# Kernel tuning notes

Hardware: AMD Instinct MI355X
Metric: run time of the kernel (lower is better)

The kernel has to match this reference:

```python
import jax, jax.numpy as jnp
import numpy as np

NUM_HEADS = 16


def setup_inputs() -> dict:
    key = jax.random.key(0)
    ks = jax.random.split(key, 3)
    B, S, E = 8, 1024, 1024
    x = jax.random.normal(ks[0], (B, S, E), dtype=jnp.float32)
    W_attn = jax.random.normal(ks[1], (E, 3 * E), dtype=jnp.float32) * (1.0 / np.sqrt(E))
    b_attn = jnp.zeros((3 * E,), dtype=jnp.float32)
    W_proj = jax.random.normal(ks[2], (E, E), dtype=jnp.float32) * (1.0 / np.sqrt(E))
    b_proj = jnp.zeros((E,), dtype=jnp.float32)
    return {"x": x, "W_attn": W_attn, "b_attn": b_attn, "W_proj": W_proj, "b_proj": b_proj}


def reference(x, W_attn, b_attn, W_proj, b_proj):
    # The module's blockwise "flash" loop implements exact causal softmax
    # attention (online softmax is mathematically identical); dropout is
    # inactive in eval mode.
    B, S, E = x.shape
    H = NUM_HEADS
    D = E // H
    qkv = x @ W_attn + b_attn  # [B,S,3E]
    q, k, v = jnp.split(qkv, 3, axis=-1)

    def split_heads(t):
        return t.reshape(B, S, H, D).transpose(0, 2, 1, 3)  # [B,H,S,D]

    q, k, v = split_heads(q), split_heads(k), split_heads(v)
    scores = jnp.einsum("bhqd,bhkd->bhqk", q, k) / jnp.sqrt(jnp.asarray(D, x.dtype))
    causal = jnp.tril(jnp.ones((S, S), dtype=bool))
    scores = jnp.where(causal, scores, -jnp.inf)
    probs = jax.nn.softmax(scores, axis=-1)
    out = jnp.einsum("bhqk,bhkd->bhqd", probs, v)  # [B,H,S,D]
    out = out.transpose(0, 2, 1, 3).reshape(B, S, E)
    return out @ W_proj + b_proj
```

## Files before the change

kernel.cpp:

```cpp
#include <hip/hip_runtime.h>
#include <hip/hip_bf16.h>
#include <stdint.h>

typedef unsigned short ushort_t;
typedef __attribute__((ext_vector_type(8))) __bf16 bf16x8;
typedef __attribute__((ext_vector_type(4))) float f32x4;

typedef const __attribute__((address_space(1))) uint32_t* gptr_t;
typedef __attribute__((address_space(3))) uint32_t* lptr_t;

__device__ __forceinline__ ushort_t f2bf(float f) {
  union { float f; uint32_t u; } x; x.f = f;
  uint32_t u = x.u;
  uint32_t r = (u + 0x7fffu + ((u >> 16) & 1u)) >> 16;
  return (ushort_t)r;
}

__device__ __forceinline__ uint32_t cvt_pk_bf16(float lo, float hi) {
  uint32_t r;
  asm("v_cvt_pk_bf16_f32 %0, %1, %2" : "=v"(r) : "v"(lo), "v"(hi));
  return r;
}

__device__ __forceinline__ void gload_lds16(const void* g, void* l) {
  __builtin_amdgcn_global_load_lds((gptr_t)g, (lptr_t)l, 16, 0, 0);
}

__global__ void cast_x(const float* __restrict__ in, ushort_t* __restrict__ out, int n) {
  const int idx = (blockIdx.x * 256 + threadIdx.x) * 4;
  if (idx < n) {
    const float4 v = *(const float4*)(in + idx);
    ushort4 o;
    o.x = f2bf(v.x); o.y = f2bf(v.y); o.z = f2bf(v.z); o.w = f2bf(v.w);
    *(ushort4*)(out + idx) = o;
  }
}

__global__ void transpose_cast(const float* __restrict__ in, ushort_t* __restrict__ out, int K, int N) {
  __shared__ ushort_t t[32][33];
  const int n0 = blockIdx.x * 32, k0 = blockIdx.y * 32;
  const int c = threadIdx.x & 31, r0 = threadIdx.x >> 5;
#pragma unroll
  for (int i = 0; i < 4; ++i) {
    const int r = r0 + i * 8;
    t[r][c] = f2bf(in[(size_t)(k0 + r) * N + n0 + c]);
  }
  __syncthreads();
#pragma unroll
  for (int i = 0; i < 4; ++i) {
    const int r = r0 + i * 8;
    out[(size_t)(n0 + r) * K + k0 + c] = t[c][r];
  }
}

template<int MODE>
__global__ __launch_bounds__(256, 2) void gemm_bt(
    const ushort_t* __restrict__ A, const ushort_t* __restrict__ Bt,
    const float* __restrict__ bias,
    ushort_t* __restrict__ Cq, ushort_t* __restrict__ Ck, ushort_t* __restrict__ Cv,
    float* __restrict__ Cf,
    int M, int N, int K, float qscale)
{
  __shared__ ushort_t As[128 * 64];
  __shared__ ushort_t Bs[128 * 64];
  const int tid = threadIdx.x;
  const int w = tid >> 6, l = tid & 63;
  const int bm = blockIdx.y * 128, bn = blockIdx.x * 128;
  const int lr = l >> 3, lp = l & 7;
  const int l16 = l & 15, lhi = l >> 4;
  const int wm = (w >> 1) * 64, wn = (w & 1) * 64;

  f32x4 acc[4][4] = {};

  for (int kt = 0; kt < K; kt += 64) {
#pragma unroll
    for (int i = 0; i < 4; ++i) {
      const int ci = i * 4 + w;
      const int row = ci * 8 + lr;
      const int sc = (lp ^ (row & 7)) * 8;
      gload_lds16(A + (size_t)(bm + row) * K + kt + sc, &As[ci * 512]);
      gload_lds16(Bt + (size_t)(bn + row) * K + kt + sc, &Bs[ci * 512]);
    }
    __syncthreads();

    bf16x8 af[4][2], bfr[4][2];
#pragma unroll
    for (int mf = 0; mf < 4; ++mf) {
      const int row = wm + mf * 16 + l16;
#pragma unroll
      for (int kf = 0; kf < 2; ++kf) {
        const int ch = (lhi + kf * 4) ^ (row & 7);
        af[mf][kf] = *(const bf16x8*)((const char*)&As[row * 64] + ch * 16);
      }
    }
#pragma unroll
    for (int nf = 0; nf < 4; ++nf) {
      const int row = wn + nf * 16 + l16;
#pragma unroll
      for (int kf = 0; kf < 2; ++kf) {
        const int ch = (lhi + kf * 4) ^ (row & 7);
        bfr[nf][kf] = *(const bf16x8*)((const char*)&Bs[row * 64] + ch * 16);
      }
    }
#pragma unroll
    for (int kf = 0; kf < 2; ++kf)
#pragma unroll
      for (int mf = 0; mf < 4; ++mf)
#pragma unroll
        for (int nf = 0; nf < 4; ++nf)
          acc[mf][nf] = __builtin_amdgcn_mfma_f32_16x16x32_bf16(
              af[mf][kf], bfr[nf][kf], acc[mf][nf], 0, 0, 0);
    __syncthreads();
  }

#pragma unroll
  for (int mf = 0; mf < 4; ++mf) {
#pragma unroll
    for (int nf = 0; nf < 4; ++nf) {
      const int col = bn + wn + nf * 16 + l16;
      const float bv = bias[col];
#pragma unroll
      for (int r = 0; r < 4; ++r) {
        const int row = bm + wm + mf * 16 + lhi * 4 + r;
        float v = acc[mf][nf][r] + bv;
        if constexpr (MODE == 1) {
          Cf[(size_t)row * N + col] = v;
        } else {
          const int region = col >> 10;
          const int hcol = col & 1023;
          const int b_ = row >> 10, s_ = row & 1023;
          const int h_ = hcol >> 6, d_ = hcol & 63;
          if (region == 2) {
            Cv[((size_t)(b_ * 16 + h_) * 64 + d_) * 1024 + s_] = f2bf(v);
          } else {
            ushort_t* base = (region == 0) ? Cq : Ck;
            if (region == 0) v *= qscale;
            base[((size_t)(b_ * 16 + h_) * 1024 + s_) * 64 + d_] = f2bf(v);
          }
        }
      }
    }
  }
}

__global__ __launch_bounds__(256, 2) void attn_kernel(
    const ushort_t* __restrict__ Q, const ushort_t* __restrict__ Kk,
    const ushort_t* __restrict__ Vt, ushort_t* __restrict__ O)
{
  __shared__ ushort_t Pl[8][32 * 68];
  const int tid = threadIdx.x;
  const int w = tid >> 6, l = tid & 63;
  const int l16 = l & 15, lhi = l >> 4;

  const int bid = blockIdx.x;
  const int bh = ((bid >> 5) << 3) | (bid & 7);
  const int p  = (bid >> 3) & 3;
  const int qtH = 7 - p, qtL = p;
  const int qbH = qtH * 128 + w * 32;
  const int qbL = qtL * 128 + w * 32;
  const int ntH = (qbH >> 6) + 1;
  const int ntL = (qbL >> 6) + 1;
  const size_t hb = (size_t)bh * (1024 * 64);
  const int b_ = bh >> 4, h_ = bh & 15;

  bf16x8 qfH[2][2], qfL[2][2];
#pragma unroll
  for (int mf = 0; mf < 2; ++mf)
#pragma unroll
    for (int kf = 0; kf < 2; ++kf) {
      qfH[mf][kf] = *(const bf16x8*)(Q + hb + (size_t)(qbH + mf * 16 + l16) * 64 + kf * 32 + lhi * 8);
      qfL[mf][kf] = *(const bf16x8*)(Q + hb + (size_t)(qbL + mf * 16 + l16) * 64 + kf * 32 + lhi * 8);
    }

  f32x4 oH[2][4] = {}, oL[2][4] = {};
  float mH[2] = {-1e30f, -1e30f}, lsH[2] = {0.0f, 0.0f};
  float mL[2] = {-1e30f, -1e30f}, lsL[2] = {0.0f, 0.0f};
  char* const pbH = (char*)&Pl[w * 2 + 0][0];
  char* const pbL = (char*)&Pl[w * 2 + 1][0];

  for (int t = 0; t < ntH; ++t) {
    const int kv0 = t * 64;

    bf16x8 kb[4][2], vb[4][2];
#pragma unroll
    for (int nf = 0; nf < 4; ++nf)
#pragma unroll
      for (int kf = 0; kf < 2; ++kf) {
        kb[nf][kf] = *(const bf16x8*)(Kk + hb + (size_t)(kv0 + nf * 16 + l16) * 64 + kf * 32 + lhi * 8);
        vb[nf][kf] = *(const bf16x8*)(Vt + hb + (size_t)(nf * 16 + l16) * 1024 + kv0 + kf * 32 + lhi * 8);
      }

    auto half = [&](const bf16x8 (&qf)[2][2], f32x4 (&o)[2][4],
                    float (&m_run)[2], float (&l_run)[2],
                    const int qbase, char* const pbase) {
      f32x4 s[2][4] = {};
#pragma unroll
      for (int nf = 0; nf < 4; ++nf)
#pragma unroll
        for (int kf = 0; kf < 2; ++kf)
#pragma unroll
          for (int mf = 0; mf < 2; ++mf)
            s[mf][nf] = __builtin_amdgcn_mfma_f32_16x16x32_bf16(kb[nf][kf], qf[mf][kf], s[mf][nf], 0, 0, 0);

      if (kv0 + 63 > qbase) {
#pragma unroll
        for (int mf = 0; mf < 2; ++mf) {
          const int q = qbase + mf * 16 + l16;
#pragma unroll
          for (int nf = 0; nf < 4; ++nf)
#pragma unroll
            for (int r = 0; r < 4; ++r) {
              const int kv = kv0 + nf * 16 + lhi * 4 + r;
              if (kv > q) s[mf][nf][r] = -1e30f;
            }
        }
      }

#pragma unroll
      for (int mf = 0; mf < 2; ++mf) {
        float lmax = -1e30f;
#pragma unroll
        for (int nf = 0; nf < 4; ++nf)
#pragma unroll
          for (int r = 0; r < 4; ++r) lmax = fmaxf(lmax, s[mf][nf][r]);
        lmax = fmaxf(lmax, __shfl_xor(lmax, 16));
        lmax = fmaxf(lmax, __shfl_xor(lmax, 32));
        const float mnew = fmaxf(m_run[mf], lmax);
        const float corr = exp2f(m_run[mf] - mnew);
        float psum = 0.0f;
#pragma unroll
        for (int nf = 0; nf < 4; ++nf)
#pragma unroll
          for (int r = 0; r < 4; ++r) {
            const float pv = exp2f(s[mf][nf][r] - mnew);
            s[mf][nf][r] = pv;
            psum += pv;
          }
        psum += __shfl_xor(psum, 16);
        psum += __shfl_xor(psum, 32);
        l_run[mf] = l_run[mf] * corr + psum;
        m_run[mf] = mnew;
#pragma unroll
        for (int nf = 0; nf < 4; ++nf) o[mf][nf] *= corr;

        const int q = mf * 16 + l16;
#pragma unroll
        for (int nf = 0; nf < 4; ++nf) {
          const uint32_t u0 = cvt_pk_bf16(s[mf][nf][0], s[mf][nf][1]);
          const uint32_t u1 = cvt_pk_bf16(s[mf][nf][2], s[mf][nf][3]);
          *(uint2*)(pbase + q * 136 + nf * 32 + lhi * 8) = make_uint2(u0, u1);
        }
      }

#pragma unroll
      for (int mf = 0; mf < 2; ++mf) {
        const int q = mf * 16 + l16;
#pragma unroll
        for (int kf = 0; kf < 2; ++kf) {
          const bf16x8 pb = *(const bf16x8*)(pbase + q * 136 + kf * 64 + lhi * 16);
#pragma unroll
          for (int nf = 0; nf < 4; ++nf)
            o[mf][nf] = __builtin_amdgcn_mfma_f32_16x16x32_bf16(vb[nf][kf], pb, o[mf][nf], 0, 0, 0);
        }
      }
    };

    half(qfH, oH, mH, lsH, qbH, pbH);
    if (t < ntL) half(qfL, oL, mL, lsL, qbL, pbL);
  }

  auto epi = [&](f32x4 (&o)[2][4], float (&l_run)[2], const int qbase) {
#pragma unroll
    for (int mf = 0; mf < 2; ++mf) {
      const float inv = 1.0f / l_run[mf];
      const int qrow = qbase + mf * 16 + l16;
      const size_t rb = ((size_t)(b_ * 1024 + qrow)) * 1024 + h_ * 64;
#pragma unroll
      for (int nf = 0; nf < 4; ++nf) {
        const uint32_t u0 = cvt_pk_bf16(o[mf][nf][0] * inv, o[mf][nf][1] * inv);
        const uint32_t u1 = cvt_pk_bf16(o[mf][nf][2] * inv, o[mf][nf][3] * inv);
        *(uint2*)(O + rb + nf * 16 + lhi * 4) = make_uint2(u0, u1);
      }
    }
  };
  epi(oH, lsH, qbH);
  epi(oL, lsL, qbL);
}

extern "C" void kernel_launch(void* const* d_in, const int* in_sizes, int n_in,
                              void* d_out, int out_size, void* d_ws, size_t ws_size,
                              hipStream_t stream) {
  const float* x      = (const float*)d_in[0];
  const float* W_attn = (const float*)d_in[1];
  const float* b_attn = (const float*)d_in[2];
  const float* W_proj = (const float*)d_in[3];
  const float* b_proj = (const float*)d_in[4];
  float* out = (float*)d_out;

  const int M = 8192;
  const int E = 1024, N3 = 3072;
  const size_t T = (size_t)M * E;

  char* p = (char*)d_ws;
  ushort_t* xb  = (ushort_t*)p; p += T * 2;
  ushort_t* Wab = (ushort_t*)p; p += (size_t)N3 * E * 2;
  ushort_t* Wpb = (ushort_t*)p; p += (size_t)E * E * 2;
  ushort_t* Qb  = (ushort_t*)p; p += T * 2;
  ushort_t* Kb  = (ushort_t*)p; p += T * 2;
  ushort_t* Vtb = (ushort_t*)p; p += T * 2;

  const float qscale = 0.125f * 1.4426950408889634f;

  cast_x<<<dim3((int)(T / 1024)), dim3(256), 0, stream>>>(x, xb, (int)T);
  transpose_cast<<<dim3(N3 / 32, E / 32), dim3(256), 0, stream>>>(W_attn, Wab, E, N3);
  transpose_cast<<<dim3(E / 32, E / 32), dim3(256), 0, stream>>>(W_proj, Wpb, E, E);
  gemm_bt<2><<<dim3(N3 / 128, M / 128), dim3(256), 0, stream>>>(
      xb, Wab, b_attn, Qb, Kb, Vtb, nullptr, M, N3, E, qscale);
  attn_kernel<<<dim3(512), dim3(256), 0, stream>>>(Qb, Kb, Vtb, xb);
  gemm_bt<1><<<dim3(E / 128, M / 128), dim3(256), 0, stream>>>(
      xb, Wpb, b_proj, nullptr, nullptr, nullptr, out, M, E, E, 1.0f);
}
```

Before: 192.0 us.

## Add 256x256 double-buffered pipelined GEMM kernel for QKV projection

Replaces the 128x128 single-buffered QKV GEMM with a new 256x256-tile kernel using 512 threads, double-buffered LDS staged in halves via global_load_lds. Loads, barriers and MFMA quads are interleaved, with setprio, so global-to-LDS traffic overlaps compute. Workgroup indices are remapped in an XCD-aware way. The costs are much larger LDS use per block (128KB), which rules out two blocks per CU, plus many barriers and hand-placed waitcnt values that must be exactly right for correctness.

Result: slower. 215.1 us (+12.0%).

```diff
diff --git a/kernel.cpp b/kernel.cpp
--- a/kernel.cpp
+++ b/kernel.cpp
@@ -25,6 +25,13 @@
 __device__ __forceinline__ void gload_lds16(const void* g, void* l) {
   __builtin_amdgcn_global_load_lds((gptr_t)g, (lptr_t)l, 16, 0, 0);
 }
+
+__device__ __forceinline__ void lgkm0_fence() {
+  asm volatile("s_waitcnt lgkmcnt(0)" ::: "memory");
+  __builtin_amdgcn_sched_barrier(0);
+}
+__device__ __forceinline__ void waitvm4() { asm volatile("s_waitcnt vmcnt(4)" ::: "memory"); }
+__device__ __forceinline__ void waitvm0() { asm volatile("s_waitcnt vmcnt(0)" ::: "memory"); }
 
 __global__ void cast_x(const float* __restrict__ in, ushort_t* __restrict__ out, int n) {
   const int idx = (blockIdx.x * 256 + threadIdx.x) * 4;
@@ -53,13 +60,174 @@
   }
 }
 
-template<int MODE>
-__global__ __launch_bounds__(256, 2) void gemm_bt(
+
+__device__ __forceinline__ void stage_half(const ushort_t* g, int ldk,
+                                           ushort_t* lds, int tid) {
+  const int r0 = tid >> 3;
+  const int ch = tid & 7;
+  const int chs = ch ^ (((tid >> 5) & 1) << 1);
+#pragma unroll
+  for (int j = 0; j < 2; ++j) {
+    const int row = j * 64 + r0;
+    gload_lds16(g + (size_t)row * ldk + chs * 8, lds + row * 64 + ch * 8);
+  }
+}
+
+__device__ __forceinline__ bf16x8 read_frag(const ushort_t* tile, int row, int kf, int lhi) {
+  const int bc = (kf * 64 + lhi * 16) ^ (((row >> 2) & 1) << 5);
+  return *(const bf16x8*)((const char*)(tile + row * 64) + bc);
+}
+
+__device__ __forceinline__ void lda4(bf16x8 (&a)[4][2], const ushort_t* At,
+                                     int mlo, int wm, int l16, int lhi) {
+#pragma unroll
+  for (int mi = 0; mi < 4; ++mi)
+#pragma unroll
+    for (int kf = 0; kf < 2; ++kf)
+      a[mi][kf] = read_frag(At, wm * 128 + (mlo + mi) * 16 + l16, kf, lhi);
+}
+
+template<int NLO>
+__device__ __forceinline__ void ldb2(bf16x8 (&b)[4][2], const ushort_t* Btile,
+                                     int wn, int l16, int lhi) {
+#pragma unroll
+  for (int ni = 0; ni < 2; ++ni)
+#pragma unroll
+    for (int kf = 0; kf < 2; ++kf)
+      b[NLO + ni][kf] = read_frag(Btile, wn * 64 + (NLO + ni) * 16 + l16, kf, lhi);
+}
+
+template<int MLO, int NLO>
+__device__ __forceinline__ void quad(f32x4 (&acc)[8][4], const bf16x8 (&a)[4][2],
+                                     const bf16x8 (&b)[4][2]) {
+  __builtin_amdgcn_s_setprio(1);
+#pragma unroll
+  for (int kf = 0; kf < 2; ++kf)
+#pragma unroll
+    for (int mi = 0; mi < 4; ++mi)
+#pragma unroll
+      for (int ni = 0; ni < 2; ++ni)
+        acc[MLO + mi][NLO + ni] = __builtin_amdgcn_mfma_f32_16x16x32_bf16(
+            a[mi][kf], b[NLO + ni][kf], acc[MLO + mi][NLO + ni], 0, 0, 0);
+  __builtin_amdgcn_s_setprio(0);
+}
+
+__global__ __launch_bounds__(512, 2) void gemm256_qkv(
     const ushort_t* __restrict__ A, const ushort_t* __restrict__ Bt,
     const float* __restrict__ bias,
     ushort_t* __restrict__ Cq, ushort_t* __restrict__ Ck, ushort_t* __restrict__ Cv,
-    float* __restrict__ Cf,
-    int M, int N, int K, float qscale)
+    int K, float qscale, int nbx)
+{
+  __shared__ ushort_t As[2][256 * 64];
+  __shared__ ushort_t Bs[2][256 * 64];
+  const int tid = threadIdx.x;
+  const int w = tid >> 6, l = tid & 63;
+  const int wm = w >> 2, wn = w & 3;
+  const int l16 = l & 15, lhi = l >> 4;
+
+  const int nwg = (int)gridDim.x;
+  const int cpx = nwg >> 3;
+  const int lt = ((int)blockIdx.x & 7) * cpx + ((int)blockIdx.x >> 3);
+  const int bm = (lt / nbx) * 256;
+  const int bn = (lt % nbx) * 256;
+
+  const ushort_t* Ag = A + (size_t)bm * K;
+  const ushort_t* Bg = Bt + (size_t)bn * K;
+
+  auto STAGE = [&](int tt, int hh) {
+    const int kt = tt * 64;
+    if (hh < 2)
+      stage_half(Ag + (size_t)(hh * 128) * K + kt, K, &As[tt & 1][hh * 128 * 64], tid);
+    else
+      stage_half(Bg + (size_t)((hh - 2) * 128) * K + kt, K, &Bs[tt & 1][(hh - 2) * 128 * 64], tid);
+  };
+
+  f32x4 acc[8][4] = {};
+  bf16x8 a[4][2], b[4][2];
+
+  const int NT = K >> 6;
+
+  STAGE(0, 0); STAGE(0, 1); STAGE(0, 2); STAGE(0, 3);
+  STAGE(1, 2); STAGE(1, 0);
+  waitvm4();
+  __builtin_amdgcn_s_barrier();
+
+  for (int t = 0; t < NT; t += 2) {
+    const bool s2 = (t + 2 < NT), s3 = (t + 3 < NT);
+    const ushort_t* A0 = &As[0][0]; const ushort_t* B0 = &Bs[0][0];
+    const ushort_t* A1 = &As[1][0]; const ushort_t* B1 = &Bs[1][0];
+
+    lda4(a, A0, 0, wm, l16, lhi); ldb2<0>(b, B0, wn, l16, lhi);
+    STAGE(t + 1, 3);
+    __builtin_amdgcn_s_barrier(); lgkm0_fence();
+    quad<0, 0>(acc, a, b);
+    __builtin_amdgcn_s_barrier();
+    ldb2<2>(b, B0, wn, l16, lhi);
+    STAGE(t + 1, 1);
+    __builtin_amdgcn_s_barrier(); lgkm0_fence();
+    quad<0, 2>(acc, a, b);
+    __builtin_amdgcn_s_barrier();
+    lda4(a, A0, 4, wm, l16, lhi);
+    if (s2) STAGE(t + 2, 2);
+    __builtin_amdgcn_s_barrier(); lgkm0_fence();
+    quad<4, 0>(acc, a, b);
+    __builtin_amdgcn_s_barrier();
+    if (s2) { STAGE(t + 2, 0); waitvm4(); } else { waitvm0(); }
+    __builtin_amdgcn_s_barrier();
+    quad<4, 2>(acc, a, b);
+    __builtin_amdgcn_s_barrier();
+
+    lda4(a, A1, 0, wm, l16, lhi); ldb2<0>(b, B1, wn, l16, lhi);
+    if (s2) STAGE(t + 2, 3);
+    __builtin_amdgcn_s_barrier(); lgkm0_fence();
+    quad<0, 0>(acc, a, b);
+    __builtin_amdgcn_s_barrier();
+    ldb2<2>(b, B1, wn, l16, lhi);
+    if (s2) STAGE(t + 2, 1);
+    __builtin_amdgcn_s_barrier(); lgkm0_fence();
+    quad<0, 2>(acc, a, b);
+    __builtin_amdgcn_s_barrier();
+    lda4(a, A1, 4, wm, l16, lhi);
+    if (s3) STAGE(t + 3, 2);
+    __builtin_amdgcn_s_barrier(); lgkm0_fence();
+    quad<4, 0>(acc, a, b);
+    __builtin_amdgcn_s_barrier();
+    if (s3) { STAGE(t + 3, 0); waitvm4(); } else if (s2) { waitvm0(); }
+    __builtin_amdgcn_s_barrier();
+    quad<4, 2>(acc, a, b);
+    __builtin_amdgcn_s_barrier();
+  }
+
+#pragma unroll
+  for (int mf = 0; mf < 8; ++mf) {
+#pragma unroll
+    for (int nf = 0; nf < 4; ++nf) {
+      const int col = bn + wn * 64 + nf * 16 + l16;
+      const float bv = bias[col];
+      const int region = col >> 10;
+      const int hcol = col & 1023;
+      const int h_ = hcol >> 6, d_ = hcol & 63;
+#pragma unroll
+      for (int r = 0; r < 4; ++r) {
+        const int row = bm + wm * 128 + mf * 16 + lhi * 4 + r;
+        float v = acc[mf][nf][r] + bv;
+        const int b_ = row >> 10, s_ = row & 1023;
+        if (region == 2) {
+          Cv[((size_t)(b_ * 16 + h_) * 64 + d_) * 1024 + s_] = f2bf(v);
+        } else {
+          ushort_t* base = (region == 0) ? Cq : Ck;
+          if (region == 0) v *= qscale;
+          base[((size_t)(b_ * 16 + h_) * 1024 + s_) * 64 + d_] = f2bf(v);
+        }
+      }
+    }
+  }
+}
+
+__global__ __launch_bounds__(256, 2) void gemm_bt(
+    const ushort_t* __restrict__ A, const ushort_t* __restrict__ Bt,
+    const float* __restrict__ bias, float* __restrict__ Cf,
+    int M, int N, int K)
 {
   __shared__ ushort_t As[128 * 64];
   __shared__ ushort_t Bs[128 * 64];
@@ -122,22 +290,7 @@
 #pragma unroll
       for (int r = 0; r < 4; ++r) {
         const int row = bm + wm + mf * 16 + lhi * 4 + r;
-        float v = acc[mf][nf][r] + bv;
-        if constexpr (MODE == 1) {
-          Cf[(size_t)row * N + col] = v;
-        } else {
-          const int region = col >> 10;
-          const int hcol = col & 1023;
-          const int b_ = row >> 10, s_ = row & 1023;
-          const int h_ = hcol >> 6, d_ = hcol & 63;
-          if (region == 2) {
-            Cv[((size_t)(b_ * 16 + h_) * 64 + d_) * 1024 + s_] = f2bf(v);
-          } else {
-            ushort_t* base = (region == 0) ? Cq : Ck;
-            if (region == 0) v *= qscale;
-            base[((size_t)(b_ * 16 + h_) * 1024 + s_) * 64 + d_] = f2bf(v);
-          }
-        }
+        Cf[(size_t)row * N + col] = acc[mf][nf][r] + bv;
       }
     }
   }
@@ -314,9 +467,9 @@
   cast_x<<<dim3((int)(T / 1024)), dim3(256), 0, stream>>>(x, xb, (int)T);
   transpose_cast<<<dim3(N3 / 32, E / 32), dim3(256), 0, stream>>>(W_attn, Wab, E, N3);
   transpose_cast<<<dim3(E / 32, E / 32), dim3(256), 0, stream>>>(W_proj, Wpb, E, E);
-  gemm_bt<2><<<dim3(N3 / 128, M / 128), dim3(256), 0, stream>>>(
-      xb, Wab, b_attn, Qb, Kb, Vtb, nullptr, M, N3, E, qscale);
+  gemm256_qkv<<<dim3((M / 256) * (N3 / 256)), dim3(512), 0, stream>>>(
+      xb, Wab, b_attn, Qb, Kb, Vtb, E, qscale, N3 / 256);
   attn_kernel<<<dim3(512), dim3(256), 0, stream>>>(Qb, Kb, Vtb, xb);
-  gemm_bt<1><<<dim3(E / 128, M / 128), dim3(256), 0, stream>>>(
-      xb, Wpb, b_proj, nullptr, nullptr, nullptr, out, M, E, E, 1.0f);
-}
+  gemm_bt<<<dim3(E / 128, M / 128), dim3(256), 0, stream>>>(
+      xb, Wpb, b_proj, out, M, E, E);
+}
```
